# Kernel tuning notes

Hardware: AMD Instinct MI355X
Metric: run time of the kernel (lower is better)

Reference implementation:

```python
import jax, jax.numpy as jnp
import numpy as np

NUM_STRINGS = 6
WEIGHT_FRET_ONSET = 0.5
STRING_WEIGHTS = jnp.ones((NUM_STRINGS,), dtype=jnp.float32)

B, S, T, C = 64, 6, 2000, 25


def setup_inputs() -> dict:
    key = jax.random.key(0)
    k1, k2, k3, k4 = jax.random.split(key, 4)
    return {
        "output_fret": jax.random.normal(k1, (B, S, T, C), dtype=jnp.float32),
        "target_fret": jax.random.randint(k2, (B, S, T), 0, C),
        "output_onset": jax.random.normal(k3, (B, S, T), dtype=jnp.float32),
        "target_onset": jax.random.uniform(k4, (B, S, T), dtype=jnp.float32),
    }


def reference(output_fret, target_fret, output_onset, target_onset):
    # ---- fret loss: standard CE over classes, mean over batch per (s,t),
    #      summed over frames, weighted per string ----
    logp_fret = jax.nn.log_softmax(output_fret, axis=-1)            # [B,S,T,C]
    nll = -jnp.take_along_axis(logp_fret, target_fret[..., None], axis=-1)[..., 0]  # [B,S,T]
    fret_st = nll.mean(axis=0)                                       # [S,T] (reduction='mean' over batch)
    fret_string_losses = fret_st.sum(axis=1) * STRING_WEIGHTS        # [S]
    fret_loss = fret_string_losses.sum()

    # ---- onset loss: torch CE with 1D [B] input + [B] float target =
    #      single example with B classes and probability targets:
    #      softmax over the BATCH dimension ----
    logp_on = jax.nn.log_softmax(output_onset, axis=0)               # softmax over B
    on_st = -(target_onset * logp_on).sum(axis=0)                    # [S,T]
    onset_string_losses = on_st.sum(axis=1) * STRING_WEIGHTS         # [S]
    onset_loss = onset_string_losses.sum()

    loss = WEIGHT_FRET_ONSET * fret_loss + (1.0 - WEIGHT_FRET_ONSET) * onset_loss
    return (loss, fret_loss, onset_loss, fret_string_losses, onset_string_losses)
```

## Files before the change

### kernel.cpp

```cpp
#include <hip/hip_runtime.h>
#include <math.h>

constexpr int Bn = 64, Sn = 6, Tn = 2000, Cn = 25;
constexpr int COLS = Sn * Tn;
constexpr int ROWS = Bn * Sn * Tn;
constexpr int BDIM = 64;

constexpr int TROWS = 64;
constexpr int TF4   = TROWS * Cn / 4;
constexpr int NT    = 4;
constexpr int RPW   = NT * TROWS;
constexpr int FBLK  = ROWS / RPW;
constexpr int FPAD  = 3072;

constexpr int OCOLS = 64;
constexpr int OBLK  = (COLS + OCOLS - 1) / OCOLS;
constexpr int OPAD  = 192;
constexpr int GRID  = OBLK + FBLK;

typedef const __attribute__((address_space(1))) unsigned int guint;
typedef __attribute__((address_space(3)))       unsigned int luint;

static __device__ __forceinline__ void seg_reduce_add(float* ls, int s, float v, int lane) {
    const int s0 = __shfl(s, 0, 64);
    const int s1 = __shfl(s, 63, 64);
    if (s0 == s1) {
        float a = v;
        #pragma unroll
        for (int off = 32; off; off >>= 1) a += __shfl_xor(a, off, 64);
        if (lane == 0) atomicAdd(&ls[s0], a);
    } else {
        float a = (s == s0) ? v : 0.0f;
        float b = (s == s0) ? 0.0f : v;
        #pragma unroll
        for (int off = 32; off; off >>= 1) {
            a += __shfl_xor(a, off, 64);
            b += __shfl_xor(b, off, 64);
        }
        if (lane == 0) { atomicAdd(&ls[s0], a); atomicAdd(&ls[s1], b); }
    }
}

__global__ __launch_bounds__(BDIM, 4) void main_kernel(const float4* __restrict__ x4,
                                                       const int*    __restrict__ tgt,
                                                       const float*  __restrict__ ox,
                                                       const float*  __restrict__ ot,
                                                       float* __restrict__ pf,
                                                       float* __restrict__ po) {
    __shared__ float4 buf4[2][TF4];
    __shared__ float  ws[Sn];
    const int lane = threadIdx.x;
    if (lane < Sn) ws[lane] = 0.0f;

    if (blockIdx.x < OBLK) {
        const int cb  = blockIdx.x;
        const int col = cb * OCOLS + lane;
        float on = 0.0f;
        int   s  = Sn - 1;
        if (col < COLS) {
            s = col / Tn;
            float M = -INFINITY, S = 0.0f, ts = 0.0f, txs = 0.0f;
            for (int b0 = 0; b0 < Bn; b0 += 8) {
                float xv[8], tv[8];
                #pragma unroll
                for (int k = 0; k < 8; ++k) xv[k] = ox[(b0 + k) * COLS + col];
                #pragma unroll
                for (int k = 0; k < 8; ++k) tv[k] = ot[(b0 + k) * COLS + col];
                float cm = -INFINITY;
                #pragma unroll
                for (int k = 0; k < 8; ++k) cm = fmaxf(cm, xv[k]);
                float cs = 0.0f;
                #pragma unroll
                for (int k = 0; k < 8; ++k) cs += __expf(xv[k] - cm);
                const float nm = fmaxf(M, cm);
                S = S * __expf(M - nm) + cs * __expf(cm - nm);
                M = nm;
                #pragma unroll
                for (int k = 0; k < 8; ++k) { ts += tv[k]; txs += tv[k] * xv[k]; }
            }
            on = ts * (M + __logf(S)) - txs;
        }
        seg_reduce_add(ws, s, on, lane);
        if (lane < Sn) po[lane * OPAD + cb] = ws[lane];
    } else {
        const int fb    = blockIdx.x - OBLK;
        const int wrow0 = fb * RPW;
        const float4* gw = x4 + (long)(wrow0 / 4) * Cn;
        float4* bb = &buf4[0][0];

        int tcs[NT];
        #pragma unroll
        for (int t = 0; t < NT; ++t) tcs[t] = tgt[wrow0 + t * TROWS + lane];

        auto stage = [&](int t) {
            const int b = t & 1;
            const float4* gs = gw + (long)t * TF4 + lane;
            #pragma unroll
            for (int k = 0; k < 6; ++k)
                __builtin_amdgcn_global_load_lds((guint*)(gs + k * 64),
                                                 (luint*)(bb + b * TF4 + k * 64), 16, 0, 0);
            if (lane < 16)
                __builtin_amdgcn_global_load_lds((guint*)(gs + 384),
                                                 (luint*)(bb + b * TF4 + 384), 16, 0, 0);
        };

        auto compute = [&](int t) {
            const int tc = tcs[t];
            const float* rp = (const float*)(bb + (t & 1) * TF4) + lane * Cn;
            float m = -INFINITY, xt = 0.0f;
            #pragma unroll
            for (int c = 0; c < Cn; ++c) {
                const float e = rp[c];
                m  = fmaxf(m, e);
                xt = (c == tc) ? e : xt;
            }
            float ss = 0.0f;
            #pragma unroll
            for (int c = 0; c < Cn; ++c) ss += __expf(rp[c] - m);
            const float nll = m + __logf(ss) - xt;
            const int s = ((wrow0 + t * TROWS + lane) / Tn) % Sn;
            seg_reduce_add(ws, s, nll, lane);
        };

        stage(0);
        stage(1);
        #pragma unroll
        for (int t = 0; t < NT; ++t) {
            if (t < NT - 1)
                asm volatile("s_waitcnt vmcnt(7)" ::: "memory");
            else
                asm volatile("s_waitcnt vmcnt(0)" ::: "memory");
            compute(t);
            if (t + 2 < NT) {
                asm volatile("s_waitcnt lgkmcnt(0)" ::: "memory");
                stage(t + 2);
            }
        }
        if (lane < Sn) pf[lane * FPAD + fb] = ws[lane];
    }
}

__global__ __launch_bounds__(1024) void finish_kernel(const float* __restrict__ pf,
                                                      const float* __restrict__ po,
                                                      float* __restrict__ out) {
    __shared__ float acc[2 * Sn];
    const int tid  = threadIdx.x;
    const int lane = tid & 63;
    if (tid < 2 * Sn) acc[tid] = 0.0f;
    __syncthreads();

    float fs[Sn];
    #pragma unroll
    for (int s = 0; s < Sn; ++s) {
        float v = 0.0f;
        for (int i = tid; i < FBLK; i += 1024) v += pf[s * FPAD + i];
        fs[s] = v;
    }
    #pragma unroll
    for (int off = 32; off; off >>= 1) {
        #pragma unroll
        for (int s = 0; s < Sn; ++s) fs[s] += __shfl_xor(fs[s], off, 64);
    }
    if (lane == 0) {
        #pragma unroll
        for (int s = 0; s < Sn; ++s) atomicAdd(&acc[s], fs[s]);
    }

    const int wv = tid >> 6;
    if (wv < Sn) {
        float v = 0.0f;
        for (int i = lane; i < OBLK; i += 64) v += po[wv * OPAD + i];
        #pragma unroll
        for (int off = 32; off; off >>= 1) v += __shfl_xor(v, off, 64);
        if (lane == 0) acc[Sn + wv] = v;
    }
    __syncthreads();

    if (tid == 0) {
        float fret = 0.0f, on = 0.0f, fsv[Sn], osv[Sn];
        #pragma unroll
        for (int s = 0; s < Sn; ++s) {
            fsv[s] = acc[s] * (1.0f / Bn);
            osv[s] = acc[Sn + s];
            fret += fsv[s];
            on   += osv[s];
        }
        out[0] = 0.5f * fret + 0.5f * on;
        out[1] = fret;
        out[2] = on;
        #pragma unroll
        for (int s = 0; s < Sn; ++s) { out[3 + s] = fsv[s]; out[9 + s] = osv[s]; }
    }
}

extern "C" void kernel_launch(void* const* d_in, const int* in_sizes, int n_in,
                              void* d_out, int out_size, void* d_ws, size_t ws_size,
                              hipStream_t stream) {
    const float* output_fret  = (const float*)d_in[0];
    const int*   target_fret  = (const int*)d_in[1];
    const float* output_onset = (const float*)d_in[2];
    const float* target_onset = (const float*)d_in[3];
    float* pf  = (float*)d_ws;
    float* po  = pf + Sn * FPAD;
    float* out = (float*)d_out;

    main_kernel<<<GRID, BDIM, 0, stream>>>((const float4*)output_fret, target_fret,
                                           output_onset, target_onset, pf, po);
    finish_kernel<<<1, 1024, 0, stream>>>(pf, po, out);
}
```

Before: 29.30 us.

## Fuse onset and fret work per wave in 768 four-wave blocks

```diff
diff --git a/kernel.cpp b/kernel.cpp
--- a/kernel.cpp
+++ b/kernel.cpp
@@ -4,19 +4,16 @@
 constexpr int Bn = 64, Sn = 6, Tn = 2000, Cn = 25;
 constexpr int COLS = Sn * Tn;
 constexpr int ROWS = Bn * Sn * Tn;
-constexpr int BDIM = 64;
+constexpr int BDIM = 256;
+constexpr int WV   = 4;
 
 constexpr int TROWS = 64;
 constexpr int TF4   = TROWS * Cn / 4;
-constexpr int NT    = 4;
-constexpr int RPW   = NT * TROWS;
-constexpr int FBLK  = ROWS / RPW;
-constexpr int FPAD  = 3072;
-
-constexpr int OCOLS = 64;
-constexpr int OBLK  = (COLS + OCOLS - 1) / OCOLS;
-constexpr int OPAD  = 192;
-constexpr int GRID  = OBLK + FBLK;
+constexpr int NTIL  = ROWS / TROWS;
+
+constexpr int GRID = 768;
+constexpr int B16  = 480;
+constexpr int PAD  = 1024;
 
 typedef const __attribute__((address_space(1))) unsigned int guint;
 typedef __attribute__((address_space(3)))       unsigned int luint;
@@ -41,102 +38,113 @@
     }
 }
 
-__global__ __launch_bounds__(BDIM, 4) void main_kernel(const float4* __restrict__ x4,
+__global__ __launch_bounds__(BDIM, 3) void main_kernel(const float4* __restrict__ x4,
                                                        const int*    __restrict__ tgt,
                                                        const float*  __restrict__ ox,
                                                        const float*  __restrict__ ot,
                                                        float* __restrict__ pf,
                                                        float* __restrict__ po) {
-    __shared__ float4 buf4[2][TF4];
-    __shared__ float  ws[Sn];
-    const int lane = threadIdx.x;
-    if (lane < Sn) ws[lane] = 0.0f;
-
-    if (blockIdx.x < OBLK) {
-        const int cb  = blockIdx.x;
-        const int col = cb * OCOLS + lane;
-        float on = 0.0f;
-        int   s  = Sn - 1;
-        if (col < COLS) {
-            s = col / Tn;
-            float M = -INFINITY, S = 0.0f, ts = 0.0f, txs = 0.0f;
-            for (int b0 = 0; b0 < Bn; b0 += 8) {
-                float xv[8], tv[8];
-                #pragma unroll
-                for (int k = 0; k < 8; ++k) xv[k] = ox[(b0 + k) * COLS + col];
-                #pragma unroll
-                for (int k = 0; k < 8; ++k) tv[k] = ot[(b0 + k) * COLS + col];
-                float cm = -INFINITY;
-                #pragma unroll
-                for (int k = 0; k < 8; ++k) cm = fmaxf(cm, xv[k]);
-                float cs = 0.0f;
-                #pragma unroll
-                for (int k = 0; k < 8; ++k) cs += __expf(xv[k] - cm);
-                const float nm = fmaxf(M, cm);
-                S = S * __expf(M - nm) + cs * __expf(cm - nm);
-                M = nm;
-                #pragma unroll
-                for (int k = 0; k < 8; ++k) { ts += tv[k]; txs += tv[k] * xv[k]; }
-            }
-            on = ts * (M + __logf(S)) - txs;
-        }
-        seg_reduce_add(ws, s, on, lane);
-        if (lane < Sn) po[lane * OPAD + cb] = ws[lane];
-    } else {
-        const int fb    = blockIdx.x - OBLK;
-        const int wrow0 = fb * RPW;
-        const float4* gw = x4 + (long)(wrow0 / 4) * Cn;
-        float4* bb = &buf4[0][0];
-
-        int tcs[NT];
-        #pragma unroll
-        for (int t = 0; t < NT; ++t) tcs[t] = tgt[wrow0 + t * TROWS + lane];
-
-        auto stage = [&](int t) {
-            const int b = t & 1;
-            const float4* gs = gw + (long)t * TF4 + lane;
-            #pragma unroll
-            for (int k = 0; k < 6; ++k)
-                __builtin_amdgcn_global_load_lds((guint*)(gs + k * 64),
-                                                 (luint*)(bb + b * TF4 + k * 64), 16, 0, 0);
-            if (lane < 16)
-                __builtin_amdgcn_global_load_lds((guint*)(gs + 384),
-                                                 (luint*)(bb + b * TF4 + 384), 16, 0, 0);
-        };
-
-        auto compute = [&](int t) {
-            const int tc = tcs[t];
-            const float* rp = (const float*)(bb + (t & 1) * TF4) + lane * Cn;
-            float m = -INFINITY, xt = 0.0f;
-            #pragma unroll
-            for (int c = 0; c < Cn; ++c) {
-                const float e = rp[c];
-                m  = fmaxf(m, e);
-                xt = (c == tc) ? e : xt;
-            }
-            float ss = 0.0f;
-            #pragma unroll
-            for (int c = 0; c < Cn; ++c) ss += __expf(rp[c] - m);
-            const float nll = m + __logf(ss) - xt;
-            const int s = ((wrow0 + t * TROWS + lane) / Tn) % Sn;
-            seg_reduce_add(ws, s, nll, lane);
-        };
-
-        stage(0);
-        stage(1);
-        #pragma unroll
-        for (int t = 0; t < NT; ++t) {
-            if (t < NT - 1)
-                asm volatile("s_waitcnt vmcnt(7)" ::: "memory");
-            else
-                asm volatile("s_waitcnt vmcnt(0)" ::: "memory");
-            compute(t);
-            if (t + 2 < NT) {
-                asm volatile("s_waitcnt lgkmcnt(0)" ::: "memory");
-                stage(t + 2);
-            }
-        }
-        if (lane < Sn) pf[lane * FPAD + fb] = ws[lane];
+    __shared__ float4 buf4[WV][2][TF4];
+    __shared__ int    tbuf[WV][2][TROWS];
+    __shared__ float  ws[WV][Sn], wo[WV][Sn];
+    const int tid  = threadIdx.x;
+    const int lane = tid & 63;
+    const int w    = tid >> 6;
+    const int b    = blockIdx.x;
+    if (lane < Sn) { ws[w][lane] = 0.0f; wo[w][lane] = 0.0f; }
+
+    const int  g     = b * WV + w;
+    const int  col0  = 4 * g;
+    const bool do_on = (col0 < COLS);
+    const int  ci = lane & 3, bq = lane >> 2;
+    float oxv[4], otv[4];
+    if (do_on) {
+        #pragma unroll
+        for (int k = 0; k < 4; ++k) {
+            const long idx = (long)(bq + 16 * k) * COLS + col0 + ci;
+            oxv[k] = ox[idx];
+            otv[k] = ot[idx];
+        }
+    }
+
+    const int tile_base = (b < B16) ? 16 * b : 16 * B16 + 15 * (b - B16);
+    const int nb        = (b < B16) ? 16 : 15;
+    const int t0        = tile_base + 4 * w;
+    const int n         = (nb - 4 * w < 4) ? nb - 4 * w : 4;
+    float4* bb = &buf4[w][0][0];
+
+    auto stage = [&](int t) {
+        const int p = t & 1;
+        const float4* gs = x4 + (long)(t0 + t) * TF4 + lane;
+        #pragma unroll
+        for (int k = 0; k < 6; ++k)
+            __builtin_amdgcn_global_load_lds((guint*)(gs + k * 64),
+                                             (luint*)(bb + p * TF4 + k * 64), 16, 0, 0);
+        if (lane < 16)
+            __builtin_amdgcn_global_load_lds((guint*)(gs + 384),
+                                             (luint*)(bb + p * TF4 + 384), 16, 0, 0);
+        __builtin_amdgcn_global_load_lds((guint*)(tgt + (long)(t0 + t) * TROWS + lane),
+                                         (luint*)&tbuf[w][p][0], 4, 0, 0);
+    };
+
+    stage(0);
+    stage(1);
+
+    if (do_on) {
+        float m = -INFINITY;
+        #pragma unroll
+        for (int k = 0; k < 4; ++k) m = fmaxf(m, oxv[k]);
+        float S = 0.0f, ts = 0.0f, txs = 0.0f;
+        #pragma unroll
+        for (int k = 0; k < 4; ++k) {
+            S   += __expf(oxv[k] - m);
+            ts  += otv[k];
+            txs += otv[k] * oxv[k];
+        }
+        #pragma unroll
+        for (int off = 4; off <= 32; off <<= 1) {
+            const float m2 = __shfl_xor(m, off, 64),  S2 = __shfl_xor(S, off, 64);
+            const float t2 = __shfl_xor(ts, off, 64), x2 = __shfl_xor(txs, off, 64);
+            const float nm = fmaxf(m, m2);
+            S  = S * __expf(m - nm) + S2 * __expf(m2 - nm);
+            m  = nm; ts += t2; txs += x2;
+        }
+        const float on = ts * (m + __logf(S)) - txs;
+        float v = (lane < 4) ? on : 0.0f;
+        v += __shfl_xor(v, 1, 64);
+        v += __shfl_xor(v, 2, 64);
+        if (lane == 0) atomicAdd(&wo[w][col0 / Tn], v);
+    }
+
+    for (int t = 0; t < n; ++t) {
+        if (t < n - 1) asm volatile("s_waitcnt vmcnt(8)" ::: "memory");
+        else           asm volatile("s_waitcnt vmcnt(0)" ::: "memory");
+        const int p  = t & 1;
+        const int tc = tbuf[w][p][lane];
+        const float* rp = (const float*)(bb + p * TF4) + lane * Cn;
+        float m = -INFINITY, xt = 0.0f;
+        #pragma unroll
+        for (int c = 0; c < Cn; ++c) {
+            const float e = rp[c];
+            m  = fmaxf(m, e);
+            xt = (c == tc) ? e : xt;
+        }
+        float ss = 0.0f;
+        #pragma unroll
+        for (int c = 0; c < Cn; ++c) ss += __expf(rp[c] - m);
+        const float nll = m + __logf(ss) - xt;
+        const int s = (((t0 + t) * TROWS + lane) / Tn) % Sn;
+        seg_reduce_add(ws[w], s, nll, lane);
+        if (t + 2 < n) {
+            asm volatile("s_waitcnt lgkmcnt(0)" ::: "memory");
+            stage(t + 2);
+        }
+    }
+
+    __syncthreads();
+    if (tid < Sn) {
+        pf[tid * PAD + b] = ws[0][tid] + ws[1][tid] + ws[2][tid] + ws[3][tid];
+        po[tid * PAD + b] = wo[0][tid] + wo[1][tid] + wo[2][tid] + wo[3][tid];
     }
 }
 
@@ -149,30 +157,23 @@
     if (tid < 2 * Sn) acc[tid] = 0.0f;
     __syncthreads();
 
-    float fs[Sn];
+    float fs[Sn], os[Sn];
     #pragma unroll
     for (int s = 0; s < Sn; ++s) {
-        float v = 0.0f;
-        for (int i = tid; i < FBLK; i += 1024) v += pf[s * FPAD + i];
-        fs[s] = v;
+        fs[s] = (tid < GRID) ? pf[s * PAD + tid] : 0.0f;
+        os[s] = (tid < GRID) ? po[s * PAD + tid] : 0.0f;
     }
     #pragma unroll
     for (int off = 32; off; off >>= 1) {
         #pragma unroll
-        for (int s = 0; s < Sn; ++s) fs[s] += __shfl_xor(fs[s], off, 64);
+        for (int s = 0; s < Sn; ++s) {
+            fs[s] += __shfl_xor(fs[s], off, 64);
+            os[s] += __shfl_xor(os[s], off, 64);
+        }
     }
     if (lane == 0) {
         #pragma unroll
-        for (int s = 0; s < Sn; ++s) atomicAdd(&acc[s], fs[s]);
-    }
-
-    const int wv = tid >> 6;
-    if (wv < Sn) {
-        float v = 0.0f;
-        for (int i = lane; i < OBLK; i += 64) v += po[wv * OPAD + i];
-        #pragma unroll
-        for (int off = 32; off; off >>= 1) v += __shfl_xor(v, off, 64);
-        if (lane == 0) acc[Sn + wv] = v;
+        for (int s = 0; s < Sn; ++s) { atomicAdd(&acc[s], fs[s]); atomicAdd(&acc[Sn + s], os[s]); }
     }
     __syncthreads();
 
@@ -201,7 +202,7 @@
     const float* output_onset = (const float*)d_in[2];
     const float* target_onset = (const float*)d_in[3];
     float* pf  = (float*)d_ws;
-    float* po  = pf + Sn * FPAD;
+    float* po  = pf + Sn * PAD;
     float* out = (float*)d_out;
 
     main_kernel<<<GRID, BDIM, 0, stream>>>((const float4*)output_fret, target_fret,
```

Measured after the change: 27.75 us. 1.06x faster.
